# Kernel optimization log

Hardware: AMD Instinct MI355X
Metric: run time of the kernel (lower is better)

## Reference

```python
import jax, jax.numpy as jnp
import numpy as np

B, IN, CB, HD, EXP, OUT, FC1 = 512, 512, 8, 256, 128, 512, 1024
CH = CB * HD            # 2048, combiner output channels
CC = IN + CH            # 2560, concat feature size
EPS = 1e-5

def _lrelu(x):
    return jnp.where(x >= 0, x, 0.2 * x)

def _bn2(x, g, b):  # BatchNorm1d on (B, C): stats over batch
    m = x.mean(0)
    v = x.var(0)
    return (x - m) * jax.lax.rsqrt(v + EPS) * g + b

def _bn3(x, g, b):  # BatchNorm1d/2d on (B, C, L): stats over (batch, length)
    m = x.mean((0, 2), keepdims=True)
    v = x.var((0, 2), keepdims=True)
    return (x - m) * jax.lax.rsqrt(v + EPS) * g[None, :, None] + b[None, :, None]

def _cmix(W, x):  # 1x1 conv over channels: (O,I) x (B,I,L) -> (B,O,L)
    return jnp.einsum('oi,bil->bol', W, x)

def setup_inputs() -> dict:
    key = jax.random.key(0)
    ks = jax.random.split(key, 16)
    def w(k, o, i):
        return jax.random.normal(k, (o, i), jnp.float32) * (1.0 / np.sqrt(i))
    u = jax.random.uniform(ks[1], (B, CB, HD, 1), jnp.float32, 1e-6, 1.0 - 1e-6)
    return {
        'x': jax.random.normal(ks[0], (B, IN), jnp.float32),
        'gumbel': -jnp.log(-jnp.log(u)),
        # combiner (Linear no-bias + BN + LeakyReLU) x3
        'cW1': w(ks[2], 2 * IN, IN), 'cg1': jnp.ones(2 * IN), 'cb1': jnp.zeros(2 * IN),
        'cW2': w(ks[3], 2 * IN, 2 * IN), 'cg2': jnp.ones(2 * IN), 'cb2': jnp.zeros(2 * IN),
        'cW3': w(ks[4], CH, 2 * IN), 'cg3': jnp.ones(CH), 'cb3': jnp.zeros(CH),
        # encoder Conv2d1x1 stack 1 -> 32 -> 64 -> 128
        'eW1': w(ks[5], EXP // 4, 1), 'eg1': jnp.ones(EXP // 4), 'eb1': jnp.zeros(EXP // 4),
        'eW2': w(ks[6], EXP // 2, EXP // 4), 'eg2': jnp.ones(EXP // 2), 'eb2': jnp.zeros(EXP // 2),
        'eW3': w(ks[7], EXP, EXP // 2), 'eg3': jnp.ones(EXP), 'eb3': jnp.zeros(EXP),
        # fc Conv1d1x1: 2560 -> 1024 (BN+lrelu), 1024 -> OUT (bias, no act)
        'fW1': w(ks[8], FC1, CC), 'fg1': jnp.ones(FC1), 'fb1': jnp.zeros(FC1),
        'fW2': w(ks[9], OUT, FC1), 'fbias2': jnp.zeros(OUT),
        # decoder Conv1d1x1: 128 -> 64 -> 32 -> 1
        'dW1': w(ks[10], EXP // 2, EXP), 'dg1': jnp.ones(EXP // 2), 'db1': jnp.zeros(EXP // 2),
        'dW2': w(ks[11], EXP // 4, EXP // 2), 'dg2': jnp.ones(EXP // 4), 'db2': jnp.zeros(EXP // 4),
        'dW3': w(ks[12], 1, EXP // 4), 'dbias3': jnp.zeros(1),
    }

def _forward(x, gumbel, cW1, cg1, cb1, cW2, cg2, cb2, cW3, cg3, cb3,
             eW1, eg1, eb1, eW2, eg2, eb2, eW3, eg3, eb3,
             fW1, fg1, fb1, fW2, fbias2,
             dW1, dg1, db1, dW2, dg2, db2, dW3, dbias3):
    # ---- combiner: logits for gumbel-softmax hard codebook selection ----
    h = _lrelu(_bn2(x @ cW1.T, cg1, cb1))
    h = _lrelu(_bn2(h @ cW2.T, cg2, cb2))
    logits = _lrelu(_bn2(h @ cW3.T, cg3, cb3)).reshape(B, CB, HD, 1)
    y = jax.nn.softmax(logits + gumbel, axis=1)  # tau = 1 (torch default)
    hard = jax.nn.one_hot(jnp.argmax(y, axis=1), CB, axis=1, dtype=y.dtype)
    w = (hard - jax.lax.stop_gradient(y) + y)[..., 0]  # (B, CB, HD) straight-through
    # weight last dim is size-1, so broadcast-mul + sum(-1) against x collapses
    # exactly to w * sum_j x_j (same math, no (B,CB,HD,IN) intermediate).
    S = x.sum(-1)          # (B,)
    S2 = (x * x).sum(-1)   # (B,)
    xs = (w * S[:, None, None]).reshape(B, CH)
    xp = (w * S2[:, None, None]).reshape(B, CH)
    z = (xs * xs - xp) * 0.5
    feat = jnp.concatenate([x, z], axis=-1)  # (B, CC)
    # ---- encoder: Conv2d1x1 stack on (B,1,1,CC) == channel mix over length CC ----
    t = feat[:, None, :]  # (B, 1, CC)
    t = _lrelu(_bn3(_cmix(eW1, t), eg1, eb1))
    t = _lrelu(_bn3(_cmix(eW2, t), eg2, eb2))
    t = _lrelu(_bn3(_cmix(eW3, t), eg3, eb3))  # (B, EXP, CC)
    # ---- fc: Conv1d over channels=CC, length=EXP ----
    t = jnp.swapaxes(t, 1, 2)  # (B, CC, EXP)
    t = _lrelu(_bn3(_cmix(fW1, t), fg1, fb1))          # (B, FC1, EXP)
    t = _cmix(fW2, t) + fbias2[None, :, None]          # (B, OUT, EXP)
    # ---- decoder: Conv1d over channels=EXP, length=OUT ----
    t = jnp.swapaxes(t, 1, 2)  # (B, EXP, OUT)
    t = _lrelu(_bn3(_cmix(dW1, t), dg1, db1))
    t = _lrelu(_bn3(_cmix(dW2, t), dg2, db2))
    t = _cmix(dW3, t) + dbias3[None, :, None]  # (B, 1, OUT)
    return t[:, 0, :]  # (B, OUT)

def reference(x, gumbel, cW1, cg1, cb1, cW2, cg2, cb2, cW3, cg3, cb3,
              eW1, eg1, eb1, eW2, eg2, eb2, eW3, eg3, eb3,
              fW1, fg1, fb1, fW2, fbias2,
              dW1, dg1, db1, dW2, dg2, db2, dW3, dbias3):
    return _forward(x, gumbel, cW1, cg1, cb1, cW2, cg2, cb2, cW3, cg3, cb3,
                    eW1, eg1, eb1, eW2, eg2, eb2, eW3, eg3, eb3,
                    fW1, fg1, fb1, fW2, fbias2,
                    dW1, dg1, db1, dW2, dg2, db2, dW3, dbias3)
```

## Files before the change

kernel.cpp:

```cpp
#include <hip/hip_runtime.h>
#include <cstddef>

#define DEV __device__ __forceinline__
DEV float lrelu(float x){ return x >= 0.0f ? x : 0.2f*x; }
typedef _Float16 f16;
typedef _Float16 f16x8 __attribute__((ext_vector_type(8)));
typedef float f32x4 __attribute__((ext_vector_type(4)));

DEV f16x8 splat8(f16 s){ f16x8 v = {s,s,s,s,s,s,s,s}; return v; }
DEV f16x8 bnl8(f16x8 v, f16x8 sc, f16x8 sh){
    f16x8 t = v*sc + sh;
    f16x8 z = splat8((f16)0.0f);
    f16x8 mx = __builtin_elementwise_max(t, z);
    f16x8 mn = __builtin_elementwise_min(t, z);
    return mx + mn*splat8((f16)0.2f);
}

DEV void gload_lds16(const f16* src, f16* dst){
    __builtin_amdgcn_global_load_lds(
        (const __attribute__((address_space(1))) void*)src,
        (__attribute__((address_space(3))) void*)dst, 16, 0, 0);
}

DEV void dma_pair(const f16* g0, const f16* g1, f16* ldsbase, int t){
    gload_lds16(g0, ldsbase + t*8);
    gload_lds16(g1, ldsbase + 2048 + t*8);
}
DEV int swz_off(int r, int g){ return r*32 + ((g ^ ((r>>1)&3))<<3); }

#define SCHED0 __builtin_amdgcn_sched_barrier(0)
#define BARRIER __builtin_amdgcn_s_barrier()

constexpr int NXPT = 512*512;

constexpr size_t O_H1  = 0;
constexpr size_t O_H2  = O_H1 + 512*1024;
constexpr size_t O_L   = O_H2 + 512*1024;
constexpr size_t O_SEL = O_L  + 512*2048;
constexpr size_t O_S   = O_SEL + 512*256;
constexpr size_t O_S2  = O_S + 512;
constexpr size_t O_VAL = O_S2 + 512;
constexpr size_t O_PRM = O_VAL + 512;
constexpr size_t P_SC1=0, P_SH1=1024, P_SC2=2048, P_SH2=3072, P_SC3=4096, P_SH3=6144;
constexpr size_t P_A1=8192, P_C1=8224, P_EW2T=8256 ;
constexpr size_t P_ACC2=18496 , P_ACC3=18624 ;
constexpr size_t P_SCE2=18880, P_SHE2=18944, P_SCE3=19008, P_SHE3=19136;
constexpr size_t P_U0=19264 , P_FTOT=19392 ;
constexpr size_t P_SCF1=20416, P_SHF1=21440;
constexpr size_t P_SCD1=22464, P_SHD1=22528, P_SCD2=22592, P_SHD2=22624;
constexpr size_t P_SCE3H=22656, P_SHE3H=22720;
constexpr size_t P_SCF1H=22784, P_SHF1H=23296;
constexpr size_t P_SCE2H=23808, P_SHE2H=23840;
constexpr size_t PRM_SIZE = 32768;
constexpr size_t O_PF  = O_H1;
constexpr size_t O_PD1 = O_H2;
constexpr size_t O_PD2 = O_H2 + 262144;
constexpr size_t O_FW1H = O_L;
constexpr size_t O_FW2H = O_L + 262144;
constexpr size_t O_ACCF = O_L + 524288;
constexpr size_t O_DW1H = O_L + 528384;
constexpr size_t O_EW3H = O_L + 532480;
constexpr size_t O_V2SS = O_L + 536576;
constexpr size_t O_U1  = O_PRM + PRM_SIZE;
constexpr size_t O_P1  = O_U1 + 512*128;
constexpr size_t O_FZT = O_P1 + 512*1024;
constexpr size_t O_V3S = O_FZT + (size_t)2048*1024;
constexpr size_t O_BIG1= O_V3S + 513*128;
constexpr size_t O_BIG2= O_BIG1 + (size_t)512*512*128/2;
constexpr size_t O_D1  = O_BIG2;
constexpr size_t O_D2  = O_BIG2 + (size_t)512*64*512;
constexpr size_t O_END = O_BIG2 + (size_t)512*1024*128/2;

#define FMA44(av,bv) do{ \
  acc[0][0]=fmaf(av.x,bv.x,acc[0][0]); acc[0][1]=fmaf(av.x,bv.y,acc[0][1]); \
  acc[0][2]=fmaf(av.x,bv.z,acc[0][2]); acc[0][3]=fmaf(av.x,bv.w,acc[0][3]); \
  acc[1][0]=fmaf(av.y,bv.x,acc[1][0]); acc[1][1]=fmaf(av.y,bv.y,acc[1][1]); \
  acc[1][2]=fmaf(av.y,bv.z,acc[1][2]); acc[1][3]=fmaf(av.y,bv.w,acc[1][3]); \
  acc[2][0]=fmaf(av.z,bv.x,acc[2][0]); acc[2][1]=fmaf(av.z,bv.y,acc[2][1]); \
  acc[2][2]=fmaf(av.z,bv.z,acc[2][2]); acc[2][3]=fmaf(av.z,bv.w,acc[2][3]); \
  acc[3][0]=fmaf(av.w,bv.x,acc[3][0]); acc[3][1]=fmaf(av.w,bv.y,acc[3][1]); \
  acc[3][2]=fmaf(av.w,bv.z,acc[3][2]); acc[3][3]=fmaf(av.w,bv.w,acc[3][3]); \
}while(0)

__global__ void k_sentinel(float* out){ out[blockIdx.x*256 + threadIdx.x] = 1.0e6f; }

__global__ __launch_bounds__(256) void k_prep(
    const float* __restrict__ fW1, const float* __restrict__ fW2,
    const float* __restrict__ dW1, const float* __restrict__ eW3,
    f16* __restrict__ fW1h, f16* __restrict__ fW2h, f16* __restrict__ dW1h,
    f16* __restrict__ eW3h, float* __restrict__ accAll)
{
    const int i = blockIdx.x*256 + threadIdx.x;
    int f = i >> 9, l = i & 511;
    fW1h[i] = (f16)fW1[(size_t)f*2560 + l];
    fW2h[i] = (f16)fW2[i];
    if (i < 8192) { dW1h[i] = (f16)dW1[i]; eW3h[i] = (f16)eW3[i]; }
    if (i < 4096) accAll[i] = 0.f;
}

__global__ __launch_bounds__(256) void k_gemm_c(
    const float* __restrict__ A, const float* __restrict__ W, float* __restrict__ C,
    int N, int K, const float* __restrict__ sc, const float* __restrict__ sh)
{
    __shared__ __align__(16) float As[16][68];
    __shared__ __align__(16) float Ws[16][68];
    const int n0 = blockIdx.x * 64, m0 = blockIdx.y * 64;
    const int t = threadIdx.x;
    const int kk = t & 15, ri = t >> 4;
    const int tx = t & 15, ty = t >> 4;
    float acc[4][4] = {{0.f,0.f,0.f,0.f},{0.f,0.f,0.f,0.f},{0.f,0.f,0.f,0.f},{0.f,0.f,0.f,0.f}};
    for (int k0 = 0; k0 < K; k0 += 16) {
        float scv = 0.f, shv = 0.f;
        if (sc) { scv = sc[k0+kk]; shv = sh[k0+kk]; }
        #pragma unroll
        for (int mm = 0; mm < 4; ++mm) {
            float v = A[(size_t)(m0 + ri + mm*16) * K + k0 + kk];
            if (sc) v = lrelu(fmaf(v, scv, shv));
            As[kk][ri + mm*16] = v;
        }
        #pragma unroll
        for (int nn = 0; nn < 4; ++nn)
            Ws[kk][ri + nn*16] = W[(size_t)(n0 + ri + nn*16) * K + k0 + kk];
        __syncthreads();
        #pragma unroll
        for (int kq = 0; kq < 16; ++kq) {
            const float4 av = *reinterpret_cast<const float4*>(&As[kq][ty*4]);
            const float4 bv = *reinterpret_cast<const float4*>(&Ws[kq][tx*4]);
            FMA44(av, bv);
        }
        __syncthreads();
    }
    #pragma unroll
    for (int i = 0; i < 4; ++i)
        #pragma unroll
        for (int j = 0; j < 4; ++j)
            C[(size_t)(m0 + ty*4 + i) * N + n0 + tx*4 + j] = acc[i][j];
}

__global__ __launch_bounds__(256) void k_stats2d_p(
    const float* __restrict__ buf, int C, float* __restrict__ part)
{
    const int t = threadIdx.x;
    const int r0 = blockIdx.x*16;
    const int c0 = blockIdx.y*1024;
    float s[4]={0.f,0.f,0.f,0.f}, s2[4]={0.f,0.f,0.f,0.f};
    for (int rr = 0; rr < 16; ++rr) {
        float4 v = *reinterpret_cast<const float4*>(buf + (size_t)(r0+rr)*C + c0 + t*4);
        s[0]+=v.x; s[1]+=v.y; s[2]+=v.z; s[3]+=v.w;
        s2[0]+=v.x*v.x; s2[1]+=v.y*v.y; s2[2]+=v.z*v.z; s2[3]+=v.w*v.w;
    }
    float* d0 = part + (size_t)blockIdx.x*2*C + c0 + t*4;
    *reinterpret_cast<float4*>(d0)     = (float4){s[0],s[1],s[2],s[3]};
    *reinterpret_cast<float4*>(d0 + C) = (float4){s2[0],s2[1],s2[2],s2[3]};
}

__global__ __launch_bounds__(256) void k_sel(
    const float* __restrict__ Lpre, const float* __restrict__ gumbel,
    const float* __restrict__ sc, const float* __restrict__ sh, int* __restrict__ sel)
{
    const int b = blockIdx.x, hd = threadIdx.x;
    float best = -3.0e38f; int bi = 0;
    #pragma unroll
    for (int cb = 0; cb < 8; ++cb) {
        int c = cb*256 + hd;
        float v = lrelu(fmaf(Lpre[(size_t)b*2048 + c], sc[c], sh[c])) + gumbel[(size_t)b*2048 + c];
        if (v > best) { best = v; bi = cb; }
    }
    sel[b*256 + hd] = bi;
}

__global__ __launch_bounds__(256) void k_val(const float* __restrict__ x,
    float* __restrict__ S, float* __restrict__ S2, float* __restrict__ val)
{
    const int b = blockIdx.x, t = threadIdx.x;
    float v0 = x[b*512 + t], v1 = x[b*512 + t + 256];
    __shared__ float ls[256], ls2[256];
    ls[t] = v0 + v1; ls2[t] = v0*v0 + v1*v1;
    __syncthreads();
    for (int off = 128; off; off >>= 1) { if (t < off) { ls[t]+=ls[t+off]; ls2[t]+=ls2[t+off]; } __syncthreads(); }
    if (t == 0) { float s = ls[0], s2 = ls2[0]; S[b]=s; S2[b]=s2; val[b]=0.5f*(s*s - s2); }
}

__global__ __launch_bounds__(256) void k_e1params(
    const float* __restrict__ S, const float* __restrict__ S2, const float* __restrict__ val,
    const float* __restrict__ eW1, const float* __restrict__ eg1, const float* __restrict__ eb1,
    float* __restrict__ A1, float* __restrict__ C1, float* __restrict__ accs )
{
    const int t = threadIdx.x;
    accs[t] = 0.f; if (t < 128) accs[256 + t] = 0.f;
    __shared__ float ls[256], ls2[256];
    float s = 0.f, s2 = 0.f;
    for (int b = t; b < 512; b += 256) {
        float vb = val[b];
        s  += S[b]  + 256.f*vb;
        s2 += S2[b] + 256.f*vb*vb;
    }
    ls[t] = s; ls2[t] = s2; __syncthreads();
    for (int off = 128; off; off >>= 1) { if (t < off) { ls[t]+=ls[t+off]; ls2[t]+=ls2[t+off]; } __syncthreads(); }
    if (t < 32) {
        const float invn = 1.0f/1310720.f;
        float mu = ls[0]*invn;
        float var = fmaxf(ls2[0]*invn - mu*mu, 0.f);
        float w = eW1[t];
        float rs = 1.0f / sqrtf(w*w*var + 1e-5f);
        float a = w * eg1[t] * rs;
        A1[t] = a; C1[t] = eb1[t] - mu*a;
    }
}

__global__ void k_wtrans2(const float* __restrict__ eW2, float* __restrict__ eW2T)
{
    const int t = threadIdx.x;
    for (int i = t; i < 2048; i += 256) { int p = i >> 5, o = i & 31; eW2T[o*64 + p] = eW2[i]; }
}

__global__ __launch_bounds__(256) void k_transpose_fz(const float* __restrict__ fW1, float* __restrict__ fzT)
{
    __shared__ float tile[64][65];
    const int z0 = blockIdx.x*64, f0 = blockIdx.y*64;
    const int j = threadIdx.x & 63, i0 = threadIdx.x >> 6;
    #pragma unroll
    for (int ii = 0; ii < 16; ++ii) {
// ... 79 lines not shown
__global__ __launch_bounds__(64) void k_wstats(
    const float* __restrict__ V, int C, float* __restrict__ acc)
{
    const int c = blockIdx.x, lane = threadIdx.x;
    float s = 0.f, s2 = 0.f;
    for (int i = lane; i < 513; i += 64) {
        float w = (i < 512) ? 256.f : 917504.f;
        float v = V[(size_t)i*C + c];
        s += w*v; s2 += w*v*v;
    }
    #pragma unroll
    for (int off = 32; off; off >>= 1) { s += __shfl_xor(s, off); s2 += __shfl_xor(s2, off); }
    if (lane == 0) { atomicAdd(&acc[c], s); atomicAdd(&acc[C + c], s2); }
}

__global__ __launch_bounds__(256) void k_stats_v2scan(const f16* __restrict__ V2x, float* __restrict__ acc2)
{
    const int t = threadIdx.x;
    const int wave = t >> 6, lane = t & 63;
    const int g = t & 7;
    const int slot = blockIdx.x*32 + (t >> 3);
    float s[8] = {0,0,0,0,0,0,0,0}, s2[8] = {0,0,0,0,0,0,0,0};
    for (int p = slot; p < NXPT; p += 2048) {
        f16x8 v = *reinterpret_cast<const f16x8*>(V2x + (size_t)p*64 + g*8);
        #pragma unroll
        for (int e = 0; e < 8; ++e) { float f = (float)v[e]; s[e] += f; s2[e] += f*f; }
    }
    #pragma unroll
    for (int off = 8; off <= 32; off <<= 1) {
        #pragma unroll
        for (int e = 0; e < 8; ++e) { s[e] += __shfl_xor(s[e], off); s2[e] += __shfl_xor(s2[e], off); }
    }
    __shared__ float red[4*128];
    if (lane < 8) {
        #pragma unroll
        for (int e = 0; e < 8; ++e) {
            red[wave*128 + lane*16 + e]     = s[e];
            red[wave*128 + lane*16 + 8 + e] = s2[e];
        }
    }
    __syncthreads();
    if (t < 128) {
        float v = red[t] + red[128 + t] + red[256 + t] + red[384 + t];
        int gg = t >> 4, k = t & 15;
        if (k < 8) atomicAdd(&acc2[gg*8 + k], v);
        else       atomicAdd(&acc2[64 + gg*8 + (k - 8)], v);
    }
}

__global__ void k_finalize(const float* __restrict__ acc, int C, float invn,
                           const float* __restrict__ g, const float* __restrict__ bb,
                           float* __restrict__ sc, float* __restrict__ sh,
                           f16* __restrict__ sch, f16* __restrict__ shh)
{
    const int idx = blockIdx.x*blockDim.x + threadIdx.x;
    if (idx < C) {
        float m = acc[idx] * invn;
        float var = fmaxf(acc[C + idx] * invn - m*m, 0.f);
        float r = 1.0f / sqrtf(var + 1e-5f);
        float s = g[idx] * r;
        float h = bb[idx] - m*s;
        sc[idx] = s; sh[idx] = h;
        if (sch) { sch[idx] = (f16)s; shh[idx] = (f16)h; }
    }
}

__global__ void k_finalize_p(const float* __restrict__ P, int C, int nPart, float invn,
                             const float* __restrict__ g, const float* __restrict__ bb,
                             float* __restrict__ sc, float* __restrict__ sh,
                             f16* __restrict__ sch, f16* __restrict__ shh)
{
    const int idx = blockIdx.x*blockDim.x + threadIdx.x;
    if (idx < C) {
        float s = 0.f, s2 = 0.f;
        for (int p = 0; p < nPart; ++p) {
            s  += P[(size_t)p*2*C + idx];
            s2 += P[(size_t)p*2*C + C + idx];
        }
        float m = s * invn;
        float var = fmaxf(s2 * invn - m*m, 0.f);
        float r = 1.0f / sqrtf(var + 1e-5f);
        float sv = g[idx] * r;
        float h = bb[idx] - m*sv;
        sc[idx] = sv; sh[idx] = h;
        if (sch) { sch[idx] = (f16)sv; shh[idx] = (f16)h; }
    }
}

__global__ __launch_bounds__(256) void k_finalize_e3(
    const float* __restrict__ P, const float* __restrict__ accw,
    const float* __restrict__ g, const float* __restrict__ bb,
    float* __restrict__ sc, float* __restrict__ sh,
    f16* __restrict__ sch, f16* __restrict__ shh)
{
    const int t = threadIdx.x, q = t & 127, h = t >> 7;
    float s = 0.f, s2 = 0.f;
    for (int p = h*1024; p < h*1024 + 1024; ++p) {
        s  += P[(size_t)p*256 + q];
        s2 += P[(size_t)p*256 + 128 + q];
    }
    __shared__ float red[2][2][128];
    red[h][0][q] = s; red[h][1][q] = s2;
    __syncthreads();
    if (t < 128) {
        float ss  = red[0][0][q] + red[1][0][q] + accw[q];
        float ss2 = red[0][1][q] + red[1][1][q] + accw[128 + q];
        const float invn = 1.0f/1310720.f;
        float m = ss * invn;
        float var = fmaxf(ss2 * invn - m*m, 0.f);
        float r = 1.0f / sqrtf(var + 1e-5f);
        float sv = g[q] * r, hh = bb[q] - m*sv;
        sc[q] = sv; sh[q] = hh; sch[q] = (f16)sv; shh[q] = (f16)hh;
    }
}

__global__ __launch_bounds__(256) void k_finalize_f(
    const float* __restrict__ P,
    const float* __restrict__ g, const float* __restrict__ bb,
    float* __restrict__ sc, float* __restrict__ sh,
    f16* __restrict__ sch, f16* __restrict__ shh)
{
    const int f = blockIdx.x*256 + threadIdx.x;
    const int fb = f >> 7, c = f & 127;
    const float* base = P + (size_t)fb*512*256 + c;
    float s = 0.f, s2 = 0.f;
    for (int b = 0; b < 512; ++b) {
        s  += base[(size_t)b*256];
        s2 += base[(size_t)b*256 + 128];
    }
    float m = s*(1.0f/65536.f);
    float var = fmaxf(s2*(1.0f/65536.f) - m*m, 0.f);
    float r = 1.0f/sqrtf(var + 1e-5f);
    float sv = g[f]*r, h = bb[f] - m*sv;
    sc[f] = sv; sh[f] = h; sch[f] = (f16)sv; shh[f] = (f16)h;
}

__global__ __launch_bounds__(256) void k_finalize_d1(
    const float* __restrict__ P,
    const float* __restrict__ g, const float* __restrict__ bb,
    float* __restrict__ sc, float* __restrict__ sh)
{
    const int t = threadIdx.x, d = t & 63, gr = t >> 6;
    float s = 0.f, s2 = 0.f;
    for (int p = gr*512; p < gr*512 + 512; ++p) {
        s  += P[(size_t)p*128 + d];
        s2 += P[(size_t)p*128 + 64 + d];
    }
    __shared__ float red[4][2][64];
    red[gr][0][d] = s; red[gr][1][d] = s2;
    __syncthreads();
    if (t < 64) {
        float ss  = red[0][0][t]+red[1][0][t]+red[2][0][t]+red[3][0][t];
        float ss2 = red[0][1][t]+red[1][1][t]+red[2][1][t]+red[3][1][t];
        float m = ss*(1.0f/262144.f);
        float var = fmaxf(ss2*(1.0f/262144.f) - m*m, 0.f);
        float r = 1.0f/sqrtf(var + 1e-5f);
        float sv = g[t]*r;
        sc[t] = sv; sh[t] = bb[t] - m*sv;
    }
}

__global__ __launch_bounds__(256) void k_mfma_e3(
    const f16* __restrict__ eW3h, const f16* __restrict__ V2x,
    const f16* __restrict__ sc2h, const f16* __restrict__ sh2h,
    f16* __restrict__ V3xT, float* __restrict__ pE3)
{
    __shared__ __align__(16) f16 As[128][76];
    __shared__ __align__(16) f16 Bs[128][76];
    __shared__ float rede[256];
    const int b = blockIdx.y, l0 = blockIdx.x * 128;
    const int t = threadIdx.x;
    const int wave = t >> 6, lane = t & 63;
    const int quad = lane >> 4, l16 = lane & 15;
    const int row = t >> 1, half = t & 1;
    #pragma unroll
    for (int c = 0; c < 4; ++c)
        *reinterpret_cast<f16x8*>(&As[row][half*32 + c*8]) =
            *reinterpret_cast<const f16x8*>(eW3h + row*64 + half*32 + c*8);
    const f16* src = V2x + ((size_t)(b*512 + l0 + row))*64 + half*32;
    #pragma unroll
    for (int c = 0; c < 4; ++c) {
        f16x8 v = *reinterpret_cast<const f16x8*>(src + c*8);
        const f16x8 csc = *reinterpret_cast<const f16x8*>(sc2h + half*32 + c*8);
        const f16x8 csh = *reinterpret_cast<const f16x8*>(sh2h + half*32 + c*8);
        *reinterpret_cast<f16x8*>(&Bs[row][half*32 + c*8]) = bnl8(v, csc, csh);
    }
    __syncthreads();
    f32x4 acc[2][8];
    #pragma unroll
    for (int i = 0; i < 2; ++i)
        #pragma unroll
        for (int j = 0; j < 8; ++j) acc[i][j] = (f32x4){0.f,0.f,0.f,0.f};
    f16x8 a0  = *reinterpret_cast<const f16x8*>(&As[32*wave + l16][quad*8]);
    f16x8 a0b = *reinterpret_cast<const f16x8*>(&As[32*wave + l16][32 + quad*8]);
    f16x8 a1  = *reinterpret_cast<const f16x8*>(&As[32*wave + 16 + l16][quad*8]);
    f16x8 a1b = *reinterpret_cast<const f16x8*>(&As[32*wave + 16 + l16][32 + quad*8]);
    #pragma unroll
    for (int j = 0; j < 8; ++j) {
        f16x8 bj  = *reinterpret_cast<const f16x8*>(&Bs[16*j + l16][quad*8]);
        f16x8 bjb = *reinterpret_cast<const f16x8*>(&Bs[16*j + l16][32 + quad*8]);
        acc[0][j] = __builtin_amdgcn_mfma_f32_16x16x32_f16(a0,  bj,  acc[0][j], 0, 0, 0);
        acc[0][j] = __builtin_amdgcn_mfma_f32_16x16x32_f16(a0b, bjb, acc[0][j], 0, 0, 0);
        acc[1][j] = __builtin_amdgcn_mfma_f32_16x16x32_f16(a1,  bj,  acc[1][j], 0, 0, 0);
        acc[1][j] = __builtin_amdgcn_mfma_f32_16x16x32_f16(a1b, bjb, acc[1][j], 0, 0, 0);
    }
    float se[8] = {0,0,0,0,0,0,0,0}, s2e[8] = {0,0,0,0,0,0,0,0};
    #pragma unroll
    for (int i = 0; i < 2; ++i) {
        #pragma unroll
        for (int r = 0; r < 4; ++r) {
            int q = 32*wave + 16*i + quad*4 + r;
            #pragma unroll
            for (int j = 0; j < 8; ++j) {
                float v = acc[i][j][r];
                V3xT[((size_t)b*128 + q)*512 + l0 + 16*j + l16] = (f16)v;
                se[i*4+r] += v; s2e[i*4+r] += v*v;
            }
        }
    }
    #pragma unroll
    for (int k = 0; k < 8; ++k) {
        se[k]  += __shfl_xor(se[k],1);  se[k]  += __shfl_xor(se[k],2);
        se[k]  += __shfl_xor(se[k],4);  se[k]  += __shfl_xor(se[k],8);
        s2e[k] += __shfl_xor(s2e[k],1); s2e[k] += __shfl_xor(s2e[k],2);
        s2e[k] += __shfl_xor(s2e[k],4); s2e[k] += __shfl_xor(s2e[k],8);
    }
    if (l16 == 0) {
        #pragma unroll
        for (int i = 0; i < 2; ++i)
            #pragma unroll
            for (int r = 0; r < 4; ++r) {
                int qq = 32*wave + 16*i + quad*4 + r;
                rede[qq] = se[i*4+r];
            }
    }
    __syncthreads();
    if (t < 128) pE3[((size_t)(blockIdx.x*512 + b))*256 + t] = rede[t];
    __syncthreads();
    if (l16 == 0) {
        #pragma unroll
        for (int i = 0; i < 2; ++i)
            #pragma unroll
            for (int r = 0; r < 4; ++r) {
                int qq = 32*wave + 16*i + quad*4 + r;
                rede[qq] = s2e[i*4+r];
            }
    }
    __syncthreads();
    if (t < 128) pE3[((size_t)(blockIdx.x*512 + b))*256 + 128 + t] = rede[t];
}

__global__ __launch_bounds__(128) void k_esupport3(
    const float* __restrict__ V2s, const float* __restrict__ sc2, const float* __restrict__ sh2,
    const float* __restrict__ eW3, float* __restrict__ V3s)
{
    const int idx = blockIdx.x, q = threadIdx.x;
    __shared__ float t2s[64];
    if (q < 64) t2s[q] = lrelu(fmaf(sc2[q], V2s[idx*64 + q], sh2[q]));
    __syncthreads();
    float s = 0.f;
    #pragma unroll
    for (int d = 0; d < 64; ++d) s = fmaf(eW3[q*64 + d], t2s[d], s);
    V3s[idx*128 + q] = s;
}

__global__ void k_u(const float* __restrict__ V3s, const float* __restrict__ sc3, const float* __restrict__ sh3,
                    float* __restrict__ u1, float* __restrict__ u0)
{
    const int idx = blockIdx.x*256 + threadIdx.x;
    if (idx < 513*128) {
        int i = idx >> 7, q = idx & 127;
        float tv = lrelu(fmaf(sc3[q], V3s[idx], sh3[q]));
        if (i < 512) u1[idx] = tv; else u0[q] = tv;
    }
}

__global__ __launch_bounds__(256) void k_mfma_fw1T(
    const f16* __restrict__ fW1h, const f16* __restrict__ V3xT,
    const f16* __restrict__ sceh, const f16* __restrict__ sheh,
    const float* __restrict__ u1, const float* __restrict__ u0,
    const float* __restrict__ P1, const float* __restrict__ Ftot,
    f16* __restrict__ out6T, float* __restrict__ pF)
{
    __shared__ __align__(16) f16 lds[24576];
    __shared__ float redf[1024];
    const int t = threadIdx.x;
    const int wave = t >> 6, lane = t & 63;
    const int quad = lane >> 4, l16 = lane & 15;
    const int n = blockIdx.x + (blockIdx.y << 3);
    const int b = (n & 7)*64 + (n >> 6);
    const int fblk = (n >> 3) & 7;
    const int f0 = fblk * 128;
    const f16* Aa = V3xT + (size_t)b*65536;
    const f16* Bb = fW1h + (size_t)f0*512;
    const int sg = (t & 3) ^ ((t >> 3) & 3);
    const size_t go0 = (size_t)(t >> 2)*512 + sg*8;
    const size_t go1 = go0 + (size_t)64*512;
    const int rA0 = 32*wave + l16, rA1 = rA0 + 16;
    const f16x8 scA0 = splat8(sceh[rA0]), shA0 = splat8(sheh[rA0]);
    const f16x8 scA1 = splat8(sceh[rA1]), shA1 = splat8(sheh[rA1]);
    const int offA0 = swz_off(rA0, quad);
    const int offA1 = swz_off(rA1, quad);
    int offB[8];
    #pragma unroll
    for (int j = 0; j < 8; ++j) offB[j] = swz_off(16*j + l16, quad);
    float p1j[8], p0j[8], u1q[8], u0q[8];
    #pragma unroll
    for (int j = 0; j < 8; ++j) {
        int f = f0 + 16*j + l16;
        p1j[j] = P1[b*1024 + f];
        p0j[j] = Ftot[f] - p1j[j];
    }
    #pragma unroll
    for (int i = 0; i < 2; ++i)
        #pragma unroll
        for (int r = 0; r < 4; ++r) {
            int q = 32*wave + 16*i + quad*4 + r;
            u1q[i*4+r] = u1[b*128 + q];
            u0q[i*4+r] = u0[q];
        }
    f32x4 acc[2][8];
    #pragma unroll
    for (int i = 0; i < 2; ++i)
        #pragma unroll
        for (int j = 0; j < 8; ++j) acc[i][j] = (f32x4){0.f,0.f,0.f,0.f};
    dma_pair(Aa + go0,      Aa + go1,      lds,               t);
    dma_pair(Bb + go0,      Bb + go1,      lds + 4096,        t);
    dma_pair(Aa + 32 + go0, Aa + 32 + go1, lds + 8192,        t);
    dma_pair(Bb + 32 + go0, Bb + 32 + go1, lds + 8192 + 4096, t);
    int m = 0;
    for (int kt = 0; kt < 16; ++kt) {
        SCHED0; BARRIER; SCHED0;
        if (kt <= 13) {
            const int mp = (m >= 1) ? m - 1 : m + 2;
            const int k0 = (kt + 2) * 32;
            dma_pair(Aa + k0 + go0, Aa + k0 + go1, lds + mp*8192,        t);
            dma_pair(Bb + k0 + go0, Bb + k0 + go1, lds + mp*8192 + 4096, t);
            asm volatile("s_waitcnt vmcnt(8)" ::: "memory");
        } else if (kt == 14) {
            asm volatile("s_waitcnt vmcnt(4)" ::: "memory");
        } else {
            asm volatile("s_waitcnt vmcnt(0)" ::: "memory");
        }
        SCHED0; BARRIER; SCHED0;
        const f16* As = lds + m*8192;
        const f16* Bs = As + 4096;
        f16x8 a0 = bnl8(*reinterpret_cast<const f16x8*>(As + offA0), scA0, shA0);
        f16x8 a1 = bnl8(*reinterpret_cast<const f16x8*>(As + offA1), scA1, shA1);
        #pragma unroll
        for (int j = 0; j < 8; ++j) {
            f16x8 bj = *reinterpret_cast<const f16x8*>(Bs + offB[j]);
            acc[0][j] = __builtin_amdgcn_mfma_f32_16x16x32_f16(a0, bj, acc[0][j], 0, 0, 0);
            acc[1][j] = __builtin_amdgcn_mfma_f32_16x16x32_f16(a1, bj, acc[1][j], 0, 0, 0);
        }
        m = (m == 2) ? 0 : m + 1;
    }
    float sj[8], s2j[8];
    #pragma unroll
    for (int j = 0; j < 8; ++j) { sj[j] = 0.f; s2j[j] = 0.f; }
    #pragma unroll
    for (int i = 0; i < 2; ++i) {
        #pragma unroll
        for (int r = 0; r < 4; ++r) {
            int q = 32*wave + 16*i + quad*4 + r;
            #pragma unroll
            for (int j = 0; j < 8; ++j) {
                int f = f0 + 16*j + l16;
                float v = acc[i][j][r] + u1q[i*4+r]*p1j[j] + u0q[i*4+r]*p0j[j];
                out6T[((size_t)b*128 + q)*1024 + f] = (f16)v;
                sj[j] += v; s2j[j] += v*v;
            }
        }
    }
    #pragma unroll
    for (int j = 0; j < 8; ++j) {
        sj[j]  += __shfl_xor(sj[j],16);  sj[j]  += __shfl_xor(sj[j],32);
        s2j[j] += __shfl_xor(s2j[j],16); s2j[j] += __shfl_xor(s2j[j],32);
    }
    if (quad == 0) {
        #pragma unroll
        for (int j = 0; j < 8; ++j) {
            redf[wave*256 + j*16 + l16]       = sj[j];
            redf[wave*256 + 128 + j*16 + l16] = s2j[j];
        }
    }
    __syncthreads();
    {
        float v = redf[t] + redf[256 + t] + redf[512 + t] + redf[768 + t];
        pF[((size_t)(fblk*512 + b))*256 + t] = v;
    }
}

__global__ __launch_bounds__(256) void k_mfma_fw2T(
    const f16* __restrict__ fW2h, const f16* __restrict__ out6T,
    const f16* __restrict__ scfh, const f16* __restrict__ shfh,
    const float* __restrict__ fbias2, f16* __restrict__ out7)
{
    __shared__ __align__(16) f16 lds[24576];
    __shared__ __align__(16) f16 scL[1024];
    __shared__ __align__(16) f16 shL[1024];
    const int t = threadIdx.x;
    const int wave = t >> 6, lane = t & 63;
    const int quad = lane >> 4, l16 = lane & 15;
    const int n = blockIdx.x + (blockIdx.y << 2);
    const int b = (n & 7)*64 + (n >> 5);
    const int o0 = ((n >> 3) & 3) * 128;
    const f16* Aa = fW2h + (size_t)o0*1024;
    const f16* Bb = out6T + (size_t)b*131072;
    const int sg = (t & 3) ^ ((t >> 3) & 3);
    const size_t go0 = (size_t)(t >> 2)*1024 + sg*8;
    const size_t go1 = go0 + (size_t)64*1024;
    const int bnO = sg*8;
    const int offA0 = swz_off(32*wave + l16, quad);
    const int offA1 = swz_off(32*wave + 16 + l16, quad);
    int offB[8];
    #pragma unroll
    for (int j = 0; j < 8; ++j) offB[j] = swz_off(16*j + l16, quad);
    float biasv[8];
    #pragma unroll
    for (int i = 0; i < 2; ++i)
        #pragma unroll
        for (int r = 0; r < 4; ++r)
            biasv[i*4+r] = fbias2[o0 + 32*wave + 16*i + quad*4 + r];
    f32x4 acc[2][8];
    #pragma unroll
    for (int i = 0; i < 2; ++i)
        #pragma unroll
        for (int j = 0; j < 8; ++j) acc[i][j] = (f32x4){0.f,0.f,0.f,0.f};
    if (t < 128) *reinterpret_cast<f16x8*>(&scL[t*8]) =
        *reinterpret_cast<const f16x8*>(scfh + t*8);
    else         *reinterpret_cast<f16x8*>(&shL[(t-128)*8]) =
        *reinterpret_cast<const f16x8*>(shfh + (t-128)*8);
    __syncthreads();
    dma_pair(Aa + go0,      Aa + go1,      lds,               t);
    dma_pair(Bb + go0,      Bb + go1,      lds + 4096,        t);
    dma_pair(Aa + 32 + go0, Aa + 32 + go1, lds + 8192,        t);
    dma_pair(Bb + 32 + go0, Bb + 32 + go1, lds + 8192 + 4096, t);
    int m = 0;
    for (int kt = 0; kt < 32; ++kt) {
        SCHED0; BARRIER; SCHED0;
        if (kt <= 29) {
            const int mp = (m >= 1) ? m - 1 : m + 2;
            const int k0 = (kt + 2) * 32;
            dma_pair(Aa + k0 + go0, Aa + k0 + go1, lds + mp*8192,        t);
            dma_pair(Bb + k0 + go0, Bb + k0 + go1, lds + mp*8192 + 4096, t);
            asm volatile("s_waitcnt vmcnt(8)" ::: "memory");
        } else if (kt == 30) {
            asm volatile("s_waitcnt vmcnt(4)" ::: "memory");
        } else {
            asm volatile("s_waitcnt vmcnt(0)" ::: "memory");
        }
        SCHED0; BARRIER; SCHED0;
        {
            f16* Bm = lds + m*8192 + 4096;
            const f16x8 csc = *reinterpret_cast<const f16x8*>(&scL[kt*32 + bnO]);
            const f16x8 csh = *reinterpret_cast<const f16x8*>(&shL[kt*32 + bnO]);
            f16x8 v0 = *reinterpret_cast<const f16x8*>(Bm + t*8);
            f16x8 v1 = *reinterpret_cast<const f16x8*>(Bm + 2048 + t*8);
            *reinterpret_cast<f16x8*>(Bm + t*8)        = bnl8(v0, csc, csh);
            *reinterpret_cast<f16x8*>(Bm + 2048 + t*8) = bnl8(v1, csc, csh);
        }
        asm volatile("s_waitcnt lgkmcnt(0)" ::: "memory");
        SCHED0; BARRIER; SCHED0;
        const f16* As = lds + m*8192;
        const f16* Bs = As + 4096;
        f16x8 a0 = *reinterpret_cast<const f16x8*>(As + offA0);
        f16x8 a1 = *reinterpret_cast<const f16x8*>(As + offA1);
        #pragma unroll
        for (int j = 0; j < 8; ++j) {
            f16x8 bj = *reinterpret_cast<const f16x8*>(Bs + offB[j]);
            acc[0][j] = __builtin_amdgcn_mfma_f32_16x16x32_f16(a0, bj, acc[0][j], 0, 0, 0);
            acc[1][j] = __builtin_amdgcn_mfma_f32_16x16x32_f16(a1, bj, acc[1][j], 0, 0, 0);
        }
        m = (m == 2) ? 0 : m + 1;
    }
    #pragma unroll
    for (int i = 0; i < 2; ++i) {
        #pragma unroll
        for (int r = 0; r < 4; ++r) {
            int o = o0 + 32*wave + 16*i + quad*4 + r;
            #pragma unroll
            for (int j = 0; j < 8; ++j) {
                int q = 16*j + l16;
                out7[((size_t)b*512 + o)*128 + q] = (f16)(acc[i][j][r] + biasv[i*4+r]);
            }
        }
    }
}

__global__ __launch_bounds__(256) void k_mfma_d1(
    const f16* __restrict__ dW1h, const f16* __restrict__ out7,
    f16* __restrict__ d1pre, float* __restrict__ pD1)
{
    __shared__ __align__(16) f16 As[64][44];
    __shared__ __align__(16) f16 Bs[128][44];
    __shared__ float redd[128];
    const int b = blockIdx.y, o0 = blockIdx.x * 128;
    const int t = threadIdx.x;
    const int wave = t >> 6, lane = t & 63;
    const int quad = lane >> 4, l16 = lane & 15;
    const int row0 = t >> 2, grp = t & 3;
    const f16* Bb = out7 + (size_t)b*65536;
    f32x4 acc[8];
    #pragma unroll
    for (int j = 0; j < 8; ++j) acc[j] = (f32x4){0.f,0.f,0.f,0.f};
    for (int k0 = 0; k0 < 128; k0 += 32) {
        *reinterpret_cast<f16x8*>(&As[row0][grp*8]) =
            *reinterpret_cast<const f16x8*>(dW1h + row0*128 + k0 + grp*8);
        #pragma unroll
        for (int p = 0; p < 2; ++p) {
            const int row = row0 + 64*p;
            *reinterpret_cast<f16x8*>(&Bs[row][grp*8]) =
                *reinterpret_cast<const f16x8*>(Bb + (size_t)(o0+row)*128 + k0 + grp*8);
        }
        __syncthreads();
        f16x8 a0 = *reinterpret_cast<const f16x8*>(&As[16*wave + l16][quad*8]);
        #pragma unroll
        for (int j = 0; j < 8; ++j) {
            f16x8 bj = *reinterpret_cast<const f16x8*>(&Bs[16*j + l16][quad*8]);
            acc[j] = __builtin_amdgcn_mfma_f32_16x16x32_f16(a0, bj, acc[j], 0, 0, 0);
        }
        __syncthreads();
    }
    float sd[4] = {0,0,0,0}, s2d[4] = {0,0,0,0};
    #pragma unroll
    for (int r = 0; r < 4; ++r) {
        int d = 16*wave + quad*4 + r;
        #pragma unroll
        for (int j = 0; j < 8; ++j) {
            int o = o0 + 16*j + l16;
            float v = acc[j][r];
            d1pre[(size_t)b*32768 + (size_t)d*512 + o] = (f16)v;
            sd[r] += v; s2d[r] += v*v;
        }
    }
    #pragma unroll
    for (int r = 0; r < 4; ++r) {
        sd[r]  += __shfl_xor(sd[r],1);  sd[r]  += __shfl_xor(sd[r],2);
        sd[r]  += __shfl_xor(sd[r],4);  sd[r]  += __shfl_xor(sd[r],8);
        s2d[r] += __shfl_xor(s2d[r],1); s2d[r] += __shfl_xor(s2d[r],2);
        s2d[r] += __shfl_xor(s2d[r],4); s2d[r] += __shfl_xor(s2d[r],8);
    }
    if (l16 == 0) {
        #pragma unroll
        for (int r = 0; r < 4; ++r) {
            int dd = 16*wave + quad*4 + r;
            redd[dd] = sd[r]; redd[64 + dd] = s2d[r];
        }
    }
    __syncthreads();
    if (t < 128) pD1[((size_t)(blockIdx.x*512 + b))*128 + t] = redd[t];
}

__global__ __launch_bounds__(256) void k_stats_cols_f32_p(
    const float* __restrict__ buf, int C, float* __restrict__ part)
{
    const int t = threadIdx.x;
    const int c = blockIdx.y*8 + (t >> 5);
    const int ol = t & 31;
    const int b0 = blockIdx.x*8;
    float s = 0.f, s2 = 0.f;
    for (int bb = 0; bb < 8; ++bb) {
        const float4* p4 = reinterpret_cast<const float4*>(buf + ((size_t)(b0+bb)*C + c)*512);
        #pragma unroll
        for (int i = 0; i < 4; ++i) {
            float4 v = p4[ol + 32*i];
            s  += v.x + v.y + v.z + v.w;
            s2 += v.x*v.x + v.y*v.y + v.z*v.z + v.w*v.w;
        }
    }
    #pragma unroll
    for (int off = 16; off; off >>= 1) { s += __shfl_xor(s, off); s2 += __shfl_xor(s2, off); }
    if (ol == 0) {
        part[(size_t)blockIdx.x*2*C + c]     = s;
        part[(size_t)blockIdx.x*2*C + C + c] = s2;
    }
}

__global__ __launch_bounds__(128) void k_gemm_d2(
    const float* __restrict__ dW2, const f16* __restrict__ d1pre,
    const float* __restrict__ scd, const float* __restrict__ shd, float* __restrict__ d2pre)
{
    __shared__ __align__(16) float As[16][36];
    __shared__ __align__(16) float Bs[16][68];
    const int n0 = blockIdx.x * 64, b = blockIdx.y;
    const int t = threadIdx.x;
    const int kk = t & 15, ri = t >> 4;
    const int qv = t & 63, kh = t >> 6;
    const int tx = t & 15, ty = t >> 4;
    float acc[4][4] = {{0.f,0.f,0.f,0.f},{0.f,0.f,0.f,0.f},{0.f,0.f,0.f,0.f},{0.f,0.f,0.f,0.f}};
    for (int k0 = 0; k0 < 64; k0 += 16) {
        #pragma unroll
        for (int mm = 0; mm < 4; ++mm)
            As[kk][ri + mm*8] = dW2[(ri + mm*8)*64 + k0 + kk];
        #pragma unroll
        for (int ki = 0; ki < 8; ++ki) {
            int d = k0 + kh + ki*2;
            float v = (float)d1pre[(size_t)b*32768 + (size_t)d*512 + n0 + qv];
            Bs[kh + ki*2][qv] = lrelu(fmaf(scd[d], v, shd[d]));
        }
        __syncthreads();
        #pragma unroll
        for (int kq = 0; kq < 16; ++kq) {
            const float4 av = *reinterpret_cast<const float4*>(&As[kq][ty*4]);
            const float4 bv = *reinterpret_cast<const float4*>(&Bs[kq][tx*4]);
            FMA44(av, bv);
        }
        __syncthreads();
    }
    #pragma unroll
    for (int i = 0; i < 4; ++i)
        #pragma unroll
        for (int j = 0; j < 4; ++j)
            d2pre[(size_t)b*16384 + (size_t)(ty*4 + i)*512 + n0 + tx*4 + j] = acc[i][j];
}

__global__ __launch_bounds__(256) void k_d3(
    const float* __restrict__ d2pre, const float* __restrict__ dW3,
    const float* __restrict__ sce, const float* __restrict__ she,
    const float* __restrict__ dbias3, float* __restrict__ out)
{
    const int idx = blockIdx.x*256 + threadIdx.x;
    const int b = idx >> 9, o = idx & 511;
    float s = dbias3[0];
    for (int e = 0; e < 32; ++e) {
        float v = d2pre[(size_t)b*16384 + e*512 + o];
        s = fmaf(dW3[e], lrelu(fmaf(v, sce[e], she[e])), s);
    }
    out[idx] = s;
}

extern "C" void kernel_launch(void* const* d_in, const int* in_sizes, int n_in,
                              void* d_out, int out_size, void* d_ws, size_t ws_size,
                              hipStream_t stream)
{
    (void)in_sizes; (void)n_in; (void)out_size;
    const float* x      = (const float*)d_in[0];
    const float* gumbel = (const float*)d_in[1];
    const float* cW1 = (const float*)d_in[2];
    const float* cg1 = (const float*)d_in[3];
    const float* cb1 = (const float*)d_in[4];
    const float* cW2 = (const float*)d_in[5];
    const float* cg2 = (const float*)d_in[6];
    const float* cb2 = (const float*)d_in[7];
    const float* cW3 = (const float*)d_in[8];
    const float* cg3 = (const float*)d_in[9];
    const float* cb3 = (const float*)d_in[10];
    const float* eW1 = (const float*)d_in[11];
    const float* eg1 = (const float*)d_in[12];
    const float* eb1 = (const float*)d_in[13];
    const float* eW2 = (const float*)d_in[14];
    const float* eg2 = (const float*)d_in[15];
    const float* eb2 = (const float*)d_in[16];
    const float* eW3 = (const float*)d_in[17];
    const float* eg3 = (const float*)d_in[18];
    const float* eb3 = (const float*)d_in[19];
    const float* fW1 = (const float*)d_in[20];
    const float* fg1 = (const float*)d_in[21];
    const float* fb1 = (const float*)d_in[22];
    const float* fW2 = (const float*)d_in[23];
    const float* fbias2 = (const float*)d_in[24];
    const float* dW1 = (const float*)d_in[25];
    const float* dg1 = (const float*)d_in[26];
    const float* db1 = (const float*)d_in[27];
    const float* dW2 = (const float*)d_in[28];
    const float* dg2 = (const float*)d_in[29];
    const float* db2 = (const float*)d_in[30];
    const float* dW3 = (const float*)d_in[31];
    const float* dbias3 = (const float*)d_in[32];
    float* out = (float*)d_out;
    float* ws  = (float*)d_ws;

    if (ws_size < O_END * sizeof(float)) {
        k_sentinel<<<1024,256,0,stream>>>(out);
        return;
    }

    float* H1  = ws + O_H1;
    float* H2  = ws + O_H2;
    float* L   = ws + O_L;
    int*   sel = (int*)(ws + O_SEL);
    float* S   = ws + O_S;
    float* S2  = ws + O_S2;
    float* val = ws + O_VAL;
    float* prm = ws + O_PRM;
    f16*   fW1h= (f16*)(ws + O_FW1H);
    f16*   fW2h= (f16*)(ws + O_FW2H);
    float* accF= ws + O_ACCF;
    f16*   dW1h= (f16*)(ws + O_DW1H);
    f16*   eW3h= (f16*)(ws + O_EW3H);
    float* V2s = ws + O_V2SS;
    float* u1  = ws + O_U1;
    float* P1  = ws + O_P1;
    float* fzT = ws + O_FZT;
    float* V3s = ws + O_V3S;
    float* pF  = ws + O_PF;
    float* pD1 = ws + O_PD1;
    float* pD2 = ws + O_PD2;
    float* p2d = ws + O_P1;
    float* pE3 = ws + O_FZT;
    f16*   V3xT= (f16*)(ws + O_BIG1);
    f16*   out7= (f16*)(ws + O_BIG1);
    f16*   out6T=(f16*)(ws + O_BIG2);
    f16*   V2x = (f16*)(ws + O_BIG2);
    f16*   d1p = (f16*)(ws + O_D1);
    float* d2p = ws + O_D2;

    const float invN_e = 1.0f/1310720.f;

    k_gemm_c<<<dim3(16,8),256,0,stream>>>(x,  cW1, H1, 1024, 512,  nullptr,     nullptr);
    k_stats2d_p<<<dim3(32,1),256,0,stream>>>(H1, 1024, p2d);
    k_finalize_p<<<4,256,0,stream>>>(p2d, 1024, 32, 1.0f/512.f, cg1, cb1,
                                     prm+P_SC1, prm+P_SH1, nullptr, nullptr);
    k_gemm_c<<<dim3(16,8),256,0,stream>>>(H1, cW2, H2, 1024, 1024, prm+P_SC1, prm+P_SH1);
    k_stats2d_p<<<dim3(32,1),256,0,stream>>>(H2, 1024, p2d);
    k_finalize_p<<<4,256,0,stream>>>(p2d, 1024, 32, 1.0f/512.f, cg2, cb2,
                                     prm+P_SC2, prm+P_SH2, nullptr, nullptr);
    k_gemm_c<<<dim3(32,8),256,0,stream>>>(H2, cW3, L,  2048, 1024, prm+P_SC2, prm+P_SH2);
    k_stats2d_p<<<dim3(32,2),256,0,stream>>>(L, 2048, p2d);
    k_finalize_p<<<8,256,0,stream>>>(p2d, 2048, 32, 1.0f/512.f, cg3, cb3,
                                     prm+P_SC3, prm+P_SH3, nullptr, nullptr);
    k_sel<<<512,256,0,stream>>>(L, gumbel, prm+P_SC3, prm+P_SH3, sel);

    k_prep<<<2048,256,0,stream>>>(fW1, fW2, dW1, eW3, fW1h, fW2h, dW1h, eW3h, accF);
    k_val<<<512,256,0,stream>>>(x, S, S2, val);
    k_e1params<<<1,256,0,stream>>>(S, S2, val, eW1, eg1, eb1, prm+P_A1, prm+P_C1, prm+P_ACC2);
    k_transpose_fz<<<dim3(32,16),256,0,stream>>>(fW1, fzT);
    k_wtrans2<<<1,256,0,stream>>>(eW2, prm+P_EW2T);
    k_ftot<<<4,256,0,stream>>>(fzT, prm+P_FTOT);
    k_p1<<<512,256,0,stream>>>(fzT, sel, P1);

    k_epass2<<<1024,256,0,stream>>>(x, prm+P_A1, prm+P_C1, prm+P_EW2T, V2x);
    k_esupport2<<<513,64,0,stream>>>(val, prm+P_A1, prm+P_C1, prm+P_EW2T, V2s);
    k_stats_v2scan<<<64,256,0,stream>>>(V2x, prm+P_ACC2);
    k_wstats<<<64,64,0,stream>>>(V2s, 64, prm+P_ACC2);
    k_finalize<<<1,256,0,stream>>>(prm+P_ACC2, 64, invN_e, eg2, eb2, prm+P_SCE2, prm+P_SHE2,
                                   (f16*)(prm+P_SCE2H), (f16*)(prm+P_SHE2H));
    k_mfma_e3<<<dim3(4,512),256,0,stream>>>(eW3h, V2x,
                                            (const f16*)(prm+P_SCE2H), (const f16*)(prm+P_SHE2H),
                                            V3xT, pE3);
    k_esupport3<<<513,128,0,stream>>>(V2s, prm+P_SCE2, prm+P_SHE2, eW3, V3s);
    k_wstats<<<128,64,0,stream>>>(V3s, 128, prm+P_ACC3);
    k_finalize_e3<<<1,256,0,stream>>>(pE3, prm+P_ACC3, eg3, eb3, prm+P_SCE3, prm+P_SHE3,
                                      (f16*)(prm+P_SCE3H), (f16*)(prm+P_SHE3H));
    k_u<<<257,256,0,stream>>>(V3s, prm+P_SCE3, prm+P_SHE3, u1, prm+P_U0);

    k_mfma_fw1T<<<dim3(8,512),256,0,stream>>>(fW1h, V3xT,
                                              (const f16*)(prm+P_SCE3H), (const f16*)(prm+P_SHE3H),
                                              u1, prm+P_U0, P1, prm+P_FTOT, out6T, pF);
    k_finalize_f<<<4,256,0,stream>>>(pF, fg1, fb1, prm+P_SCF1, prm+P_SHF1,
                                     (f16*)(prm+P_SCF1H), (f16*)(prm+P_SHF1H));
    k_mfma_fw2T<<<dim3(4,512),256,0,stream>>>(fW2h, out6T,
                                              (const f16*)(prm+P_SCF1H), (const f16*)(prm+P_SHF1H),
                                              fbias2, out7);

    k_mfma_d1<<<dim3(4,512),256,0,stream>>>(dW1h, out7, d1p, pD1);
    k_finalize_d1<<<1,256,0,stream>>>(pD1, dg1, db1, prm+P_SCD1, prm+P_SHD1);
    k_gemm_d2<<<dim3(8,512),128,0,stream>>>(dW2, d1p, prm+P_SCD1, prm+P_SHD1, d2p);
    k_stats_cols_f32_p<<<dim3(64,4),256,0,stream>>>(d2p, 32, pD2);
    k_finalize_p<<<1,32,0,stream>>>(pD2, 32, 64, 1.0f/262144.f, dg2, db2,
                                    prm+P_SCD2, prm+P_SHD2, nullptr, nullptr);
    k_d3<<<1024,256,0,stream>>>(d2p, dW3, prm+P_SCD2, prm+P_SHD2, dbias3, out);
}
```

Before: 925.9 us.

## Fuse decoder d1 GEMM into fc2 epilogue and d2 stats into GEMM

```diff
diff --git a/kernel.cpp b/kernel.cpp
--- a/kernel.cpp
+++ b/kernel.cpp
@@ -67,7 +67,7 @@
 constexpr size_t O_V3S = O_FZT + (size_t)2048*1024;
 constexpr size_t O_BIG1= O_V3S + 513*128;
 constexpr size_t O_BIG2= O_BIG1 + (size_t)512*512*128/2;
-constexpr size_t O_D1  = O_BIG2;
+constexpr size_t O_D1  = O_BIG1;
 constexpr size_t O_D2  = O_BIG2 + (size_t)512*64*512;
 constexpr size_t O_END = O_BIG2 + (size_t)512*1024*128/2;
 
@@ -453,6 +453,32 @@
     if (t < 64) {
         float ss  = red[0][0][t]+red[1][0][t]+red[2][0][t]+red[3][0][t];
         float ss2 = red[0][1][t]+red[1][1][t]+red[2][1][t]+red[3][1][t];
+        float m = ss*(1.0f/262144.f);
+        float var = fmaxf(ss2*(1.0f/262144.f) - m*m, 0.f);
+        float r = 1.0f/sqrtf(var + 1e-5f);
+        float sv = g[t]*r;
+        sc[t] = sv; sh[t] = bb[t] - m*sv;
+    }
+}
+
+__global__ __launch_bounds__(256) void k_finalize_d2(
+    const float* __restrict__ P,
+    const float* __restrict__ g, const float* __restrict__ bb,
+    float* __restrict__ sc, float* __restrict__ sh)
+{
+    const int t = threadIdx.x, e = t & 31, gr = t >> 5;
+    float s = 0.f, s2 = 0.f;
+    for (int p = gr*512; p < gr*512 + 512; ++p) {
+        s  += P[(size_t)p*64 + e];
+        s2 += P[(size_t)p*64 + 32 + e];
+    }
+    __shared__ float red[8][2][32];
+    red[gr][0][e] = s; red[gr][1][e] = s2;
+    __syncthreads();
+    if (t < 32) {
+        float ss = 0.f, ss2 = 0.f;
+        #pragma unroll
+        for (int k2 = 0; k2 < 8; ++k2) { ss += red[k2][0][t]; ss2 += red[k2][1][t]; }
         float m = ss*(1.0f/262144.f);
         float var = fmaxf(ss2*(1.0f/262144.f) - m*m, 0.f);
         float r = 1.0f/sqrtf(var + 1e-5f);
@@ -695,7 +721,8 @@
 __global__ __launch_bounds__(256) void k_mfma_fw2T(
     const f16* __restrict__ fW2h, const f16* __restrict__ out6T,
     const f16* __restrict__ scfh, const f16* __restrict__ shfh,
-    const float* __restrict__ fbias2, f16* __restrict__ out7)
+    const float* __restrict__ fbias2, const f16* __restrict__ dW1h,
+    f16* __restrict__ d1pre, float* __restrict__ pD1)
 {
     __shared__ __align__(16) f16 lds[24576];
     __shared__ __align__(16) f16 scL[1024];
@@ -775,115 +802,89 @@
         }
         m = (m == 2) ? 0 : m + 1;
     }
+    __syncthreads();
+    f16* ot = lds;
+    float* redp = (float*)(lds + 128*136);
     #pragma unroll
     for (int i = 0; i < 2; ++i) {
         #pragma unroll
         for (int r = 0; r < 4; ++r) {
-            int o = o0 + 32*wave + 16*i + quad*4 + r;
+            int ob = 32*wave + 16*i + quad*4 + r;
             #pragma unroll
-            for (int j = 0; j < 8; ++j) {
-                int q = 16*j + l16;
-                out7[((size_t)b*512 + o)*128 + q] = (f16)(acc[i][j][r] + biasv[i*4+r]);
+            for (int j = 0; j < 8; ++j)
+                ot[ob*136 + 16*j + l16] = (f16)(acc[i][j][r] + biasv[i*4+r]);
+        }
+    }
+    __syncthreads();
+    f32x4 dacc[4][2];
+    #pragma unroll
+    for (int dt = 0; dt < 4; ++dt)
+        #pragma unroll
+        for (int u = 0; u < 2; ++u) dacc[dt][u] = (f32x4){0.f,0.f,0.f,0.f};
+    #pragma unroll
+    for (int kq = 0; kq < 4; ++kq) {
+        f16x8 bfr[2];
+        #pragma unroll
+        for (int u = 0; u < 2; ++u) {
+            int ob = (2*wave + u)*16 + l16;
+            bfr[u] = *reinterpret_cast<const f16x8*>(ot + ob*136 + kq*32 + quad*8);
+        }
+        #pragma unroll
+        for (int dt = 0; dt < 4; ++dt) {
+            f16x8 afr = *reinterpret_cast<const f16x8*>(dW1h + (dt*16 + l16)*128 + kq*32 + quad*8);
+            #pragma unroll
+            for (int u = 0; u < 2; ++u)
+                dacc[dt][u] = __builtin_amdgcn_mfma_f32_16x16x32_f16(afr, bfr[u], dacc[dt][u], 0, 0, 0);
+        }
+    }
+    float sd = 0.f, s2d = 0.f;
+    float sdv[16], s2dv[16];
+    #pragma unroll
+    for (int dt = 0; dt < 4; ++dt) {
+        #pragma unroll
+        for (int ri = 0; ri < 4; ++ri) {
+            int d = dt*16 + quad*4 + ri;
+            float vs = 0.f, v2s = 0.f;
+            #pragma unroll
+            for (int u = 0; u < 2; ++u) {
+                int o = o0 + (2*wave + u)*16 + l16;
+                float v = dacc[dt][u][ri];
+                d1pre[(size_t)b*32768 + (size_t)d*512 + o] = (f16)v;
+                vs += v; v2s += v*v;
             }
-        }
-    }
-}
-
-__global__ __launch_bounds__(256) void k_mfma_d1(
-    const f16* __restrict__ dW1h, const f16* __restrict__ out7,
-    f16* __restrict__ d1pre, float* __restrict__ pD1)
-{
-    __shared__ __align__(16) f16 As[64][44];
-    __shared__ __align__(16) f16 Bs[128][44];
-    __shared__ float redd[128];
-    const int b = blockIdx.y, o0 = blockIdx.x * 128;
-    const int t = threadIdx.x;
-    const int wave = t >> 6, lane = t & 63;
-    const int quad = lane >> 4, l16 = lane & 15;
-    const int row0 = t >> 2, grp = t & 3;
-    const f16* Bb = out7 + (size_t)b*65536;
-    f32x4 acc[8];
-    #pragma unroll
-    for (int j = 0; j < 8; ++j) acc[j] = (f32x4){0.f,0.f,0.f,0.f};
-    for (int k0 = 0; k0 < 128; k0 += 32) {
-        *reinterpret_cast<f16x8*>(&As[row0][grp*8]) =
-            *reinterpret_cast<const f16x8*>(dW1h + row0*128 + k0 + grp*8);
-        #pragma unroll
-        for (int p = 0; p < 2; ++p) {
-            const int row = row0 + 64*p;
-            *reinterpret_cast<f16x8*>(&Bs[row][grp*8]) =
-                *reinterpret_cast<const f16x8*>(Bb + (size_t)(o0+row)*128 + k0 + grp*8);
-        }
-        __syncthreads();
-        f16x8 a0 = *reinterpret_cast<const f16x8*>(&As[16*wave + l16][quad*8]);
-        #pragma unroll
-        for (int j = 0; j < 8; ++j) {
-            f16x8 bj = *reinterpret_cast<const f16x8*>(&Bs[16*j + l16][quad*8]);
-            acc[j] = __builtin_amdgcn_mfma_f32_16x16x32_f16(a0, bj, acc[j], 0, 0, 0);
-        }
-        __syncthreads();
-    }
-    float sd[4] = {0,0,0,0}, s2d[4] = {0,0,0,0};
-    #pragma unroll
-    for (int r = 0; r < 4; ++r) {
-        int d = 16*wave + quad*4 + r;
-        #pragma unroll
-        for (int j = 0; j < 8; ++j) {
-            int o = o0 + 16*j + l16;
-            float v = acc[j][r];
-            d1pre[(size_t)b*32768 + (size_t)d*512 + o] = (f16)v;
-            sd[r] += v; s2d[r] += v*v;
-        }
-    }
-    #pragma unroll
-    for (int r = 0; r < 4; ++r) {
-        sd[r]  += __shfl_xor(sd[r],1);  sd[r]  += __shfl_xor(sd[r],2);
-        sd[r]  += __shfl_xor(sd[r],4);  sd[r]  += __shfl_xor(sd[r],8);
-        s2d[r] += __shfl_xor(s2d[r],1); s2d[r] += __shfl_xor(s2d[r],2);
-        s2d[r] += __shfl_xor(s2d[r],4); s2d[r] += __shfl_xor(s2d[r],8);
-    }
+            vs  += __shfl_xor(vs,1);  vs  += __shfl_xor(vs,2);
+            vs  += __shfl_xor(vs,4);  vs  += __shfl_xor(vs,8);
+            v2s += __shfl_xor(v2s,1); v2s += __shfl_xor(v2s,2);
+            v2s += __shfl_xor(v2s,4); v2s += __shfl_xor(v2s,8);
+            sdv[dt*4+ri] = vs; s2dv[dt*4+ri] = v2s;
+        }
+    }
+    (void)sd; (void)s2d;
     if (l16 == 0) {
         #pragma unroll
-        for (int r = 0; r < 4; ++r) {
-            int dd = 16*wave + quad*4 + r;
-            redd[dd] = sd[r]; redd[64 + dd] = s2d[r];
-        }
-    }
-    __syncthreads();
-    if (t < 128) pD1[((size_t)(blockIdx.x*512 + b))*128 + t] = redd[t];
-}
-
-__global__ __launch_bounds__(256) void k_stats_cols_f32_p(
-    const float* __restrict__ buf, int C, float* __restrict__ part)
-{
-    const int t = threadIdx.x;
-    const int c = blockIdx.y*8 + (t >> 5);
-    const int ol = t & 31;
-    const int b0 = blockIdx.x*8;
-    float s = 0.f, s2 = 0.f;
-    for (int bb = 0; bb < 8; ++bb) {
-        const float4* p4 = reinterpret_cast<const float4*>(buf + ((size_t)(b0+bb)*C + c)*512);
-        #pragma unroll
-        for (int i = 0; i < 4; ++i) {
-            float4 v = p4[ol + 32*i];
-            s  += v.x + v.y + v.z + v.w;
-            s2 += v.x*v.x + v.y*v.y + v.z*v.z + v.w*v.w;
-        }
-    }
-    #pragma unroll
-    for (int off = 16; off; off >>= 1) { s += __shfl_xor(s, off); s2 += __shfl_xor(s2, off); }
-    if (ol == 0) {
-        part[(size_t)blockIdx.x*2*C + c]     = s;
-        part[(size_t)blockIdx.x*2*C + C + c] = s2;
+        for (int dt = 0; dt < 4; ++dt)
+            #pragma unroll
+            for (int ri = 0; ri < 4; ++ri) {
+                int d = dt*16 + quad*4 + ri;
+                redp[wave*128 + d]      = sdv[dt*4+ri];
+                redp[wave*128 + 64 + d] = s2dv[dt*4+ri];
+            }
+    }
+    __syncthreads();
+    if (t < 128) {
+        float v = redp[t] + redp[128 + t] + redp[256 + t] + redp[384 + t];
+        pD1[(size_t)n*128 + t] = v;
     }
 }
 
 __global__ __launch_bounds__(128) void k_gemm_d2(
     const float* __restrict__ dW2, const f16* __restrict__ d1pre,
-    const float* __restrict__ scd, const float* __restrict__ shd, float* __restrict__ d2pre)
+    const float* __restrict__ scd, const float* __restrict__ shd,
+    float* __restrict__ d2pre, float* __restrict__ pD2)
 {
     __shared__ __align__(16) float As[16][36];
     __shared__ __align__(16) float Bs[16][68];
+    __shared__ float sred[64];
     const int n0 = blockIdx.x * 64, b = blockIdx.y;
     const int t = threadIdx.x;
     const int kk = t & 15, ri = t >> 4;
@@ -910,10 +911,25 @@
         __syncthreads();
     }
     #pragma unroll
-    for (int i = 0; i < 4; ++i)
-        #pragma unroll
-        for (int j = 0; j < 4; ++j)
-            d2pre[(size_t)b*16384 + (size_t)(ty*4 + i)*512 + n0 + tx*4 + j] = acc[i][j];
+    for (int i = 0; i < 4; ++i) {
+        float s = 0.f, s2 = 0.f;
+        #pragma unroll
+        for (int j = 0; j < 4; ++j) {
+            float v = acc[i][j];
+            d2pre[(size_t)b*16384 + (size_t)(ty*4 + i)*512 + n0 + tx*4 + j] = v;
+            s += v; s2 += v*v;
+        }
+        s  += __shfl_xor(s,1);  s  += __shfl_xor(s,2);
+        s  += __shfl_xor(s,4);  s  += __shfl_xor(s,8);
+        s2 += __shfl_xor(s2,1); s2 += __shfl_xor(s2,2);
+        s2 += __shfl_xor(s2,4); s2 += __shfl_xor(s2,8);
+        if (tx == 0) {
+            int e = ty*4 + i;
+            sred[e] = s; sred[32 + e] = s2;
+        }
+    }
+    __syncthreads();
+    if (t < 64) pD2[((size_t)(blockIdx.y*8 + blockIdx.x))*64 + t] = sred[t];
 }
 
 __global__ __launch_bounds__(256) void k_d3(
@@ -1001,7 +1017,6 @@
     float* p2d = ws + O_P1;
     float* pE3 = ws + O_FZT;
     f16*   V3xT= (f16*)(ws + O_BIG1);
-    f16*   out7= (f16*)(ws + O_BIG1);
     f16*   out6T=(f16*)(ws + O_BIG2);
     f16*   V2x = (f16*)(ws + O_BIG2);
     f16*   d1p = (f16*)(ws + O_D1);
@@ -1053,13 +1068,10 @@
                                      (f16*)(prm+P_SCF1H), (f16*)(prm+P_SHF1H));
     k_mfma_fw2T<<<dim3(4,512),256,0,stream>>>(fW2h, out6T,
                                               (const f16*)(prm+P_SCF1H), (const f16*)(prm+P_SHF1H),
-                                              fbias2, out7);
-
-    k_mfma_d1<<<dim3(4,512),256,0,stream>>>(dW1h, out7, d1p, pD1);
+                                              fbias2, dW1h, d1p, pD1);
+
     k_finalize_d1<<<1,256,0,stream>>>(pD1, dg1, db1, prm+P_SCD1, prm+P_SHD1);
-    k_gemm_d2<<<dim3(8,512),128,0,stream>>>(dW2, d1p, prm+P_SCD1, prm+P_SHD1, d2p);
-    k_stats_cols_f32_p<<<dim3(64,4),256,0,stream>>>(d2p, 32, pD2);
-    k_finalize_p<<<1,32,0,stream>>>(pD2, 32, 64, 1.0f/262144.f, dg2, db2,
-                                    prm+P_SCD2, prm+P_SHD2, nullptr, nullptr);
+    k_gemm_d2<<<dim3(8,512),128,0,stream>>>(dW2, d1p, prm+P_SCD1, prm+P_SHD1, d2p, pD2);
+    k_finalize_d2<<<1,256,0,stream>>>(pD2, dg2, db2, prm+P_SCD2, prm+P_SHD2);
     k_d3<<<1024,256,0,stream>>>(d2p, dW3, prm+P_SCD2, prm+P_SHD2, dbias3, out);
 }
```

New measurement: 941.8 us. About the same (+1.7%).
